# Optimization experiments

Measured on AMD Instinct MI355X. Metric: run time of the kernel, lower is better.

The kernel has to match this reference:

```python
import jax, jax.numpy as jnp
import numpy as np

N = 20000      # nodes per node type
E = 320000     # edges per relation (avg degree 16)
D_IN = 128     # input node feature dim
H = 256        # hidden_channels
L = 2          # num_layers
G = 32         # graphs in batch
NUM_REL = 6
# relation order: (vuln,ast,vuln),(vuln,dfg,vuln),(vuln,aligned,patch),(patch,aligned,vuln),(patch,ast,patch),(patch,dfg,patch)
REL_SRC = (0, 0, 0, 1, 1, 1)  # 0=vuln, 1=patch
REL_DST = (0, 0, 1, 0, 1, 1)


def setup_inputs() -> dict:
    key = jax.random.key(0)
    ks = jax.random.split(key, 12)
    s_in = 1.0 / np.sqrt(D_IN)
    s_h = 1.0 / np.sqrt(H)
    return {
        'x_vuln': jax.random.normal(ks[0], (N, D_IN), jnp.float32),
        'x_patch': jax.random.normal(ks[1], (N, D_IN), jnp.float32),
        'W_emb': jax.random.normal(ks[2], (2, D_IN, H), jnp.float32) * s_in,
        'b_emb': jnp.zeros((2, H), jnp.float32),
        'W_l': jax.random.normal(ks[3], (L, NUM_REL, H, H), jnp.float32) * s_h,
        'b_l': jnp.zeros((L, NUM_REL, H), jnp.float32),
        'W_r': jax.random.normal(ks[4], (L, NUM_REL, H, H), jnp.float32) * s_h,
        'gamma': jnp.ones((L, 2, H), jnp.float32),
        'beta': jnp.zeros((L, 2, H), jnp.float32),
        'W_out': jax.random.normal(ks[5], (2 * H, 1), jnp.float32) * (1.0 / np.sqrt(2 * H)),
        'b_out': jnp.zeros((1,), jnp.float32),
        'edge_index': jax.random.randint(ks[6], (NUM_REL, 2, E), 0, N, jnp.int64),
        'batch_vuln': jnp.sort(jax.random.randint(ks[7], (N,), 0, G, jnp.int64)),
        'batch_patch': jnp.sort(jax.random.randint(ks[8], (N,), 0, G, jnp.int64)),
        'num_graphs': G,
    }


def _segment_mean(data, seg, num):
    s = jax.ops.segment_sum(data, seg, num_segments=num)
    c = jax.ops.segment_sum(jnp.ones((data.shape[0], 1), data.dtype), seg, num_segments=num)
    return s / jnp.maximum(c, 1.0)


def _batchnorm(x, gamma, beta, eps=1e-5):
    m = x.mean(axis=0)
    v = x.var(axis=0)  # biased, matches torch BN normalization
    return (x - m) * jax.lax.rsqrt(v + eps) * gamma + beta


def reference(x_vuln, x_patch, W_emb, b_emb, W_l, b_l, W_r, gamma, beta,
              W_out, b_out, edge_index, batch_vuln, batch_patch, num_graphs):
    # per-type input projection
    xs = [x_vuln @ W_emb[0] + b_emb[0], x_patch @ W_emb[1] + b_emb[1]]
    n = [x_vuln.shape[0], x_patch.shape[0]]
    for i in range(L):
        prev = xs
        acc = [jnp.zeros((n[t], H), xs[0].dtype) for t in range(2)]
        cnt = [0, 0]
        for r in range(NUM_REL):  # fixed small structural loop over relations
            st, dt = REL_SRC[r], REL_DST[r]
            src, dst = edge_index[r, 0], edge_index[r, 1]
            agg = _segment_mean(xs[st][src], dst, n[dt])  # [n_dst, H] mean over in-neighbors
            out = agg @ W_l[i, r] + b_l[i, r] + xs[dt] @ W_r[i, r]  # SAGEConv
            acc[dt] = acc[dt] + out
            cnt[dt] += 1
        xs = [acc[t] / cnt[t] for t in range(2)]  # HeteroConv aggr='mean'
        xs = [jax.nn.relu(_batchnorm(xs[t], gamma[i, t], beta[i, t])) for t in range(2)]
        if i > 0:
            xs = [xs[t] + prev[t] for t in range(2)]  # residual
    gv = _segment_mean(xs[0], batch_vuln, num_graphs)   # global_mean_pool
    gp = _segment_mean(xs[1], batch_patch, num_graphs)
    cat = jnp.concatenate([gv, gp], axis=1)            # [G, 2H]
    return jax.nn.sigmoid(cat @ W_out + b_out)         # [G, 1]
```

## Files before the change

### kernel.cpp

```cpp
#include <hip/hip_runtime.h>
#include <math.h>

#define NODES 20000
#define EDGES 320000
#define DIN 128
#define HID 256
#define NGRAPH 32
#define NREL 6
#define STR 1088
#define NRG 32
#define RGN 625
#define BCAP 11264
#define BINSLC 4000

typedef __attribute__((ext_vector_type(8))) short bf16x8;
typedef __attribute__((ext_vector_type(8))) unsigned short u16x8;
typedef __attribute__((ext_vector_type(4))) unsigned short u16x4;
typedef __attribute__((ext_vector_type(4))) float f32x4;

__device__ __forceinline__ float bf2f(unsigned short u) {
  return __uint_as_float(((unsigned)u) << 16);
}
__device__ __forceinline__ unsigned short f2bf(float f) {
  unsigned u = __float_as_uint(f);
  unsigned r = (u + 0x7fffu + ((u >> 16) & 1u)) >> 16;
  return (unsigned short)r;
}

__device__ __forceinline__ unsigned char f2fp8(float f) {
  unsigned u = __float_as_uint(f);
  unsigned s = (u >> 24) & 0x80u;
  unsigned a = u & 0x7fffffffu;
  if (a < 0x3c800000u) return (unsigned char)s;
  if (a > 0x43e00000u) a = 0x43e00000u;
  a += 0x7ffffu + ((a >> 20) & 1u);
  unsigned em = (a >> 20) - (120u << 3);
  if (em > 0x7eu) em = 0x7eu;
  return (unsigned char)(s | em);
}
__device__ __forceinline__ float fp82f(unsigned b) {
  unsigned u = ((b & 0x80u) << 24) | ((b & 0x7fu) << 20);
  return __uint_as_float(u) * __uint_as_float(0x7B800000u);
}
__device__ __forceinline__ void fp8x4_acc(unsigned v, float& a0, float& a1, float& a2,
                                          float& a3) {
#if __has_builtin(__builtin_amdgcn_cvt_pk_f32_fp8)
  typedef float f32x2 __attribute__((ext_vector_type(2)));
  f32x2 lo = __builtin_amdgcn_cvt_pk_f32_fp8((int)v, false);
  f32x2 hi = __builtin_amdgcn_cvt_pk_f32_fp8((int)v, true);
  a0 += lo[0];
  a1 += lo[1];
  a2 += hi[0];
  a3 += hi[1];
#else
  a0 += fp82f(v & 0xffu);
  a1 += fp82f((v >> 8) & 0xffu);
  a2 += fp82f((v >> 16) & 0xffu);
  a3 += fp82f(v >> 24);
#endif
}

#define GLDS(g, l)                                                            \
  __builtin_amdgcn_global_load_lds(                                           \
      (const __attribute__((address_space(1))) void*)(g),                     \
      (__attribute__((address_space(3))) void*)(l), 16, 0, 0)

__global__ __launch_bounds__(256) void k_bin(const int* __restrict__ edges,
                                             unsigned* __restrict__ bucket,
                                             int* __restrict__ gcur) {
  __shared__ unsigned buf[NRG][256];
  __shared__ int cnt[NRG];
  __shared__ int gbaseL[NRG];
  int rel = blockIdx.y;
  for (int i = threadIdx.x; i < NRG; i += 256) cnt[i] = 0;
  __syncthreads();
  const int* srcp = edges + (size_t)rel * 2 * EDGES;
  const int* dstp = srcp + EDGES;
  int base = blockIdx.x * BINSLC;
  for (int i = base + threadIdx.x; i < base + BINSLC; i += 256) {
    int d = __builtin_nontemporal_load(&dstp[i]);
    int s = __builtin_nontemporal_load(&srcp[i]);
    int rg = (unsigned)d / RGN;
    int dl = d - rg * RGN;
    int p = atomicAdd(&cnt[rg], 1);
    if (p < 256) buf[rg][p] = ((unsigned)dl << 16) | (unsigned)s;
  }
  __syncthreads();
  if (threadIdx.x < NRG) {
    int n = min(cnt[threadIdx.x], 256);
    gbaseL[threadIdx.x] = atomicAdd(&gcur[rel * NRG + threadIdx.x], n);
    cnt[threadIdx.x] = n;
  }
  __syncthreads();
  for (int b = 0; b < NRG; ++b) {
    int n = cnt[b];
    unsigned* gb = bucket + ((size_t)rel * NRG + b) * BCAP + gbaseL[b];
    for (int k = threadIdx.x; k < n; k += 256) gb[k] = buf[b][k];
  }
}

__global__ void k_base(const int* __restrict__ gcur, int* __restrict__ gbase,
                       int* __restrict__ rowoff) {
  int t = threadIdx.x;
  for (int rel = 0; rel < NREL; ++rel) {
    int v = (t < NRG) ? gcur[rel * NRG + t] : 0;
    int x = v;
#pragma unroll
    for (int s = 1; s < NRG; s <<= 1) {
      int u = __shfl_up(x, s, 64);
      if (t >= s) x += u;
    }
    if (t < NRG) gbase[rel * NRG + t] = x - v;
    if (t == 0) rowoff[rel * (NODES + 1) + NODES] = EDGES;
  }
}

__global__ __launch_bounds__(256) void k_scat2(const unsigned* __restrict__ bucket,
                                               const int* __restrict__ gcur,
                                               const int* __restrict__ gbase,
                                               int* __restrict__ rowoff,
                                               unsigned short* __restrict__ csr16) {
  __shared__ int h[RGN];
  __shared__ int wsum[4];
  int rg = blockIdx.x, rel = blockIdx.y;
  int nE = gcur[rel * NRG + rg];
  int base = gbase[rel * NRG + rg];
  for (int i = threadIdx.x; i < RGN; i += 256) h[i] = 0;
  __syncthreads();
  const unsigned* bk = bucket + ((size_t)rel * NRG + rg) * BCAP;
  for (int i = threadIdx.x; i < nE; i += 256) atomicAdd(&h[bk[i] >> 16], 1);
  __syncthreads();
  int t = threadIdx.x, lane = t & 63, w = t >> 6;
  int i0 = t * 3;
  int v0 = (i0 < RGN) ? h[i0] : 0;
  int v1 = (i0 + 1 < RGN) ? h[i0 + 1] : 0;
  int v2 = (i0 + 2 < RGN) ? h[i0 + 2] : 0;
  int ts = v0 + v1 + v2;
  int x = ts;
#pragma unroll
  for (int s = 1; s < 64; s <<= 1) {
    int u = __shfl_up(x, s, 64);
    if (lane >= s) x += u;
  }
  if (lane == 63) wsum[w] = x;
  __syncthreads();
  int wb = 0;
  for (int k = 0; k < w; ++k) wb += wsum[k];
  int excl = base + wb + x - ts;
  int* ro = rowoff + rel * (NODES + 1) + rg * RGN;
  __syncthreads();
  if (i0 < RGN) {
    ro[i0] = excl;
    h[i0] = excl;
  }
  if (i0 + 1 < RGN) {
    ro[i0 + 1] = excl + v0;
    h[i0 + 1] = excl + v0;
  }
  if (i0 + 2 < RGN) {
    ro[i0 + 2] = excl + v0 + v1;
    h[i0 + 2] = excl + v0 + v1;
  }
  __syncthreads();
  unsigned short* cs = csr16 + (size_t)rel * EDGES;
  for (int i = threadIdx.x; i < nE; i += 256) {
    unsigned e = bk[i];
    int p = atomicAdd(&h[e >> 16], 1);
    cs[p] = (unsigned short)(e & 0xffffu);
  }
}

__global__ void k_xcvt(const float* __restrict__ xv, const float* __restrict__ xp,
                       unsigned short* __restrict__ xbf) {
  int idx = blockIdx.x * 256 + threadIdx.x;
  const int ND = NODES * DIN;
  int e0 = idx * 4;
  if (e0 >= 2 * ND) return;
  const float* s = (e0 < ND) ? (xv + e0) : (xp + e0 - ND);
  float4 v = *(const float4*)s;
  u16x4 o;
  o[0] = f2bf(v.x);
  o[1] = f2bf(v.y);
  o[2] = f2bf(v.z);
  o[3] = f2bf(v.w);
  *(u16x4*)(xbf + e0) = o;
}

__global__ void k_wtrans(const float* __restrict__ W_l, const float* __restrict__ W_r,
                         unsigned short* __restrict__ Wt) {
  const int rels[2][3] = {{0, 1, 3}, {2, 4, 5}};
  int kt = blockIdx.x, nt = blockIdx.y, ld = blockIdx.z;
  int layer = ld >> 1, dt = ld & 1;
  __shared__ float sh[16][17];
  int k0 = kt * 16, n0 = nt * 16;
  int seg = k0 >> 8, kk0 = k0 & 255;
  int tx = threadIdx.x, ty = threadIdx.y;
  float v;
  if (seg < 3) {
    v = W_l[(((size_t)layer * NREL + rels[dt][seg]) * HID + kk0 + ty) * HID + n0 + tx];
  } else {
    v = 0.f;
    for (int j = 0; j < 3; ++j)
      v += W_r[(((size_t)layer * NREL + rels[dt][j]) * HID + kk0 + ty) * HID + n0 + tx];
  }
  sh[ty][tx] = v;
  __syncthreads();
  Wt[((size_t)ld * HID + n0 + ty) * 1024 + k0 + tx] = f2bf(sh[tx][ty]);
}

__global__ void k_wembt(const float* __restrict__ W_emb, unsigned short* __restrict__ Wet) {
  int kt = blockIdx.x, nt = blockIdx.y, t = blockIdx.z;
  __shared__ float sh[16][17];
  int k0 = kt * 16, n0 = nt * 16;
  int tx = threadIdx.x, ty = threadIdx.y;
  sh[ty][tx] = W_emb[((size_t)t * DIN + k0 + ty) * HID + n0 + tx];
  __syncthreads();
  Wet[((size_t)t * HID + n0 + ty) * DIN + k0 + tx] = f2bf(sh[tx][ty]);
}

__global__ void k_bsum(const float* __restrict__ b_l, float* __restrict__ bsum) {
  const int rels[2][3] = {{0, 1, 3}, {2, 4, 5}};
  int idx = blockIdx.x * 256 + threadIdx.x;
  if (idx >= 1024) return;
  int layer = idx >> 9, dt = (idx >> 8) & 1, c = idx & 255;
  float s = 0.f;
  for (int j = 0; j < 3; ++j) s += b_l[(layer * NREL + rels[dt][j]) * HID + c];
  bsum[idx] = s;
}

__global__ __launch_bounds__(256) void k_agg(const unsigned char* __restrict__ xs8,
                                             unsigned short* __restrict__ a0,
                                             unsigned short* __restrict__ a1,
                                             const int* __restrict__ rowoff,
                                             const unsigned short* __restrict__ csr16) {
  const int dt_of[6] = {0, 0, 1, 0, 1, 1};
  const int seg_of[6] = {0, 1, 0, 2, 1, 2};
  int x = blockIdx.x;
  int st = x >> 2, rq = x & 3;
  int rel = st * 3 + blockIdx.z;
  int dt = dt_of[rel], seg = seg_of[rel];
  const unsigned char* src = xs8 + (size_t)st * NODES * 256;
  unsigned short* dstb = (dt == 0 ? a0 : a1) + seg * 256;
  int lane16 = threadIdx.x & 15;
  int rsub = threadIdx.x >> 4;
  unsigned coff = (unsigned)lane16 * 16u;
  const int* ro = rowoff + rel * (NODES + 1);
  const unsigned short* lst = csr16 + (size_t)rel * EDGES;
  int rlim = rq * 5000 + 5000;
  int rbase = rq * 5000 + blockIdx.y * 32;
#define LD(s) (*(const uint4*)(src + ((unsigned)(s) * 256u + coff)))
#define ACCV(v)                                  \
  {                                              \
    fp8x4_acc((v).x, ac[0], ac[1], ac[2], ac[3]);   \
    fp8x4_acc((v).y, ac[4], ac[5], ac[6], ac[7]);   \
    fp8x4_acc((v).z, ac[8], ac[9], ac[10], ac[11]); \
    fp8x4_acc((v).w, ac[12], ac[13], ac[14], ac[15]); \
  }
  int row = rbase + rsub;
  int o0 = 0, o1 = 0;
  if (row < rlim) {
    o0 = ro[row];
    o1 = ro[row + 1];
  }
#pragma unroll 1
  for (int pass = 0; pass < 2; ++pass) {
    int nrow = row + 16;
    int p0 = 0, p1 = 0;
    if (pass < 1 && nrow < rlim) {
      p0 = ro[nrow];
      p1 = ro[nrow + 1];
    }
    if (row < rlim) {
      float ac[16] = {};
      int nb = o1 - o0;
      int nfull = nb >> 2;
      int j = o0;
      if (nfull > 0) {
        unsigned idx[4];
#pragma unroll
        for (int b = 0; b < 4; ++b) idx[b] = (unsigned)lst[j + b];
#pragma unroll 1
        for (int f = 1;; ++f) {
          uint4 v0 = LD(idx[0]), v1 = LD(idx[1]), v2 = LD(idx[2]), v3 = LD(idx[3]);
          j += 4;
          bool more = (f < nfull);
          if (more) {
#pragma unroll
            for (int b = 0; b < 4; ++b) idx[b] = (unsigned)lst[j + b];
          }
          ACCV(v0);
          ACCV(v1);
          ACCV(v2);
          ACCV(v3);
          if (!more) break;
        }
      }
      int rem = nb & 3;
      if (rem & 2) {
        unsigned i0 = lst[j], i1 = lst[j + 1];
        uint4 v0 = LD(i0), v1 = LD(i1);
        ACCV(v0);
        ACCV(v1);
        j += 2;
      }
      if (rem & 1) {
        uint4 v0 = LD((unsigned)lst[j]);
        ACCV(v0);
      }
      float inv = nb ? 1.f / (float)nb : 0.f;
      u16x8 oa, ob;
#pragma unroll
      for (int e = 0; e < 8; ++e) {
        oa[e] = f2bf(ac[e] * inv);
        ob[e] = f2bf(ac[8 + e] * inv);
      }
      unsigned short* dp = dstb + (size_t)row * STR + lane16 * 16;
      *(u16x8*)dp = oa;
      *(u16x8*)(dp + 8) = ob;
    }
    row = nrow;
    o0 = p0;
    o1 = p1;
  }
#undef LD
#undef ACCV
}

template <int K, int AS, int OUTMODE>
__global__ __launch_bounds__(256) void k_mfma(const unsigned short* __restrict__ Abase,
                                              const unsigned short* __restrict__ Btbase,
                                              const float* __restrict__ biasbase,
                                              float* __restrict__ Crawbase,
                                              unsigned short* __restrict__ Cbfbase,
                                              unsigned char* __restrict__ X8base,
                                              float* __restrict__ statsbase) {
  int bid = blockIdx.x;
  int sel = blockIdx.y;
  int bm_i = (bid & 7) + 8 * (bid >> 5);
  int bn_i = (bid >> 3) & 3;
  if (bm_i >= 157) return;
  const unsigned short* A = Abase + (size_t)sel * NODES * AS;
  const unsigned short* Bt = Btbase + (size_t)sel * 256 * K;
  const float* bias = biasbase + sel * 256;
  const int bm = bm_i * 128, bn = bn_i * 64;
  __shared__ unsigned short As[2][128 * 64];
  __shared__ unsigned short Bs[2][64 * 64];
  const int tid = threadIdx.x, lane = tid & 63, w = tid >> 6;
  const int wr = w >> 1, wc = w & 1;
  const int srow = lane >> 3;
  const int schunk = lane & 7;
  const unsigned char* gA[4];
  const unsigned char* gB[2];
#pragma unroll
  for (int c = 0; c < 4; ++c) {
    int lr = 32 * c + w * 8 + srow;
    int r = bm + lr;
    if (r >= NODES) r = NODES - 1;
    gA[c] = (const unsigned char*)A + (size_t)r * AS * 2 + ((schunk ^ (lr & 7)) * 16);
  }
#pragma unroll
  for (int c = 0; c < 2; ++c) {
    int lr = 32 * c + w * 8 + srow;
    gB[c] = (const unsigned char*)Bt + (size_t)(bn + lr) * K * 2 + ((schunk ^ (lr & 7)) * 16);
  }

  auto stage = [&](int b, int k0) {
#pragma unroll
    for (int c = 0; c < 4; ++c) GLDS(gA[c] + 2 * k0, (char*)As[b] + c * 4096 + w * 1024);
#pragma unroll
    for (int c = 0; c < 2; ++c) GLDS(gB[c] + 2 * k0, (char*)Bs[b] + c * 4096 + w * 1024);
  };

  f32x4 acc[4][2] = {};
  stage(0, 0);
  __syncthreads();
  int cur = 0;
  for (int k0 = 0; k0 < K; k0 += 64) {
    if (k0 + 64 < K) stage(cur ^ 1, k0 + 64);
    const unsigned short* Ab = As[cur];
    const unsigned short* Bb = Bs[cur];
#pragma unroll
    for (int ks = 0; ks < 2; ++ks) {
      const int ci = ks * 4 + (lane >> 4);
      bf16x8 bfr[2];
#pragma unroll
      for (int n = 0; n < 2; ++n) {
        int rb = wc * 32 + n * 16 + (lane & 15);
        bfr[n] = *(const bf16x8*)((const char*)Bb + rb * 128 + ((ci ^ (rb & 7)) * 16));
      }
#pragma unroll
      for (int m = 0; m < 4; ++m) {
        int ra = wr * 64 + m * 16 + (lane & 15);
        bf16x8 afr = *(const bf16x8*)((const char*)Ab + ra * 128 + ((ci ^ (ra & 7)) * 16));
        acc[m][0] =
            __builtin_amdgcn_mfma_f32_16x16x32_bf16(afr, bfr[0], acc[m][0], 0, 0, 0);
        acc[m][1] =
            __builtin_amdgcn_mfma_f32_16x16x32_bf16(afr, bfr[1], acc[m][1], 0, 0, 0);
      }
    }
    __syncthreads();
    cur ^= 1;
  }

#pragma unroll
  for (int n = 0; n < 2; ++n) {
    int col = bn + wc * 32 + n * 16 + (lane & 15);
    float bv = bias[col];
    float s = 0.f, s2 = 0.f;
#pragma unroll
    for (int m = 0; m < 4; ++m) {
#pragma unroll
      for (int q = 0; q < 4; ++q) {
        int row = bm + wr * 64 + m * 16 + ((lane >> 4) * 4) + q;
        if (row < NODES) {
          float v = acc[m][n][q] + bv;
          if (OUTMODE == 0) {
            Crawbase[(size_t)sel * NODES * 256 + (size_t)row * 256 + col] = v;
            s += v;
            s2 = fmaf(v, v, s2);
          } else {
            Cbfbase[(size_t)sel * NODES * STR + (size_t)row * STR + col] = f2bf(v);
            X8base[(size_t)sel * NODES * 256 + (size_t)row * 256 + col] = f2fp8(v);
          }
        }
      }
    }
    if (OUTMODE == 0) {
      s += __shfl_xor(s, 16);
      s += __shfl_xor(s, 32);
      s2 += __shfl_xor(s2, 16);
      s2 += __shfl_xor(s2, 32);
      if (lane < 16) {
        float* stats = statsbase + sel * 512;
        atomicAdd(&stats[col], s);
        atomicAdd(&stats[256 + col], s2);
      }
    }
  }
}

__global__ __launch_bounds__(256) void k_bnapply(const float* __restrict__ rawbase,
                                                 const float* __restrict__ statsbase,
                                                 const float* __restrict__ gammabase,
                                                 const float* __restrict__ betabase,
                                                 unsigned short* __restrict__ outbase,
                                                 unsigned char* __restrict__ out8base) {
  int idx = blockIdx.x * 256 + threadIdx.x;
  if (idx >= NODES * 256) return;
  int dt = blockIdx.y;
  const float* raw = rawbase + (size_t)dt * NODES * 256;
  const float* stats = statsbase + dt * 512;
  const float* gamma = gammabase + dt * 256;
  const float* beta = betabase + dt * 256;
  unsigned short* out = outbase + (size_t)dt * NODES * STR;
  unsigned char* out8 = out8base + (size_t)dt * NODES * 256;
  int c = idx & 255;
  int rrow = idx >> 8;
  const float inv3 = 1.f / 3.f;
  float m = stats[c] * (inv3 / NODES);
  float ex2 = stats[256 + c] * (inv3 * inv3 / NODES);
  float var = ex2 - m * m;
  float v = (raw[idx] * inv3 - m) * rsqrtf(var + 1e-5f) * gamma[c] + beta[c];
  v = fmaxf(v, 0.f);
  out[(size_t)rrow * STR + c] = f2bf(v);
  out8[idx] = f2fp8(v);
}

__global__ __launch_bounds__(256) void k_pool(const float* __restrict__ rawbase,
                                              const float* __restrict__ statsbase,
                                              const float* __restrict__ gammabase,
                                              const float* __restrict__ betabase,
                                              const unsigned short* __restrict__ prevbase,
                                              const int* __restrict__ batch_v,
                                              const int* __restrict__ batch_p,
                                              float* __restrict__ pooledbase,
                                              float* __restrict__ gcntbase) {
  int dt = blockIdx.y;
  const float* raw = rawbase + (size_t)dt * NODES * 256;
  const float* stats = statsbase + dt * 512;
  const float* gamma = gammabase + dt * 256;
  const float* beta = betabase + dt * 256;
  const unsigned short* prev = prevbase + (size_t)dt * NODES * STR;
  const int* batch = dt ? batch_p : batch_v;
  float* pooled = pooledbase + dt * NGRAPH * 256;
  float* gcnt = gcntbase + dt * NGRAPH;
  int c = threadIdx.x;
  int rows_per = (NODES + gridDim.x - 1) / gridDim.x;
  int r0 = blockIdx.x * rows_per;
  int r1 = min(NODES, r0 + rows_per);
  if (r0 >= NODES) return;
  const float inv3 = 1.f / 3.f;
  float m = stats[c] * (inv3 / NODES);
  float ex2 = stats[256 + c] * (inv3 * inv3 / NODES);
  float rs = rsqrtf(ex2 - m * m + 1e-5f) * gamma[c];
  float bt = beta[c];
  float s = 0.f;
  int curg = batch[r0];
  for (int r = r0; r < r1; ++r) {
    int g = batch[r];
    if (g != curg) {
      atomicAdd(&pooled[curg * 256 + c], s);
      s = 0.f;
      curg = g;
    }
    float v = fmaxf((raw[(size_t)r * 256 + c] * inv3 - m) * rs + bt, 0.f) +
              bf2f(prev[(size_t)r * STR + c]);
    s += v;
  }
  atomicAdd(&pooled[curg * 256 + c], s);
  if (c == 0) {
    int cn = 0;
    int cg = batch[r0];
    for (int r = r0; r < r1; ++r) {
      int g = batch[r];
      if (g != cg) {
        atomicAdd(&gcnt[cg], (float)cn);
        cn = 0;
        cg = g;
      }
      cn++;
    }
    atomicAdd(&gcnt[cg], (float)cn);
  }
}

__global__ __launch_bounds__(256) void k_final(const float* __restrict__ pooled,
                                               const float* __restrict__ gcnt,
                                               const float* __restrict__ Wout,
                                               const float* __restrict__ bout,
                                               float* __restrict__ out) {
  int g = blockIdx.x;
  int h = threadIdx.x;
  float cv = fmaxf(gcnt[g], 1.f);
  float cp = fmaxf(gcnt[NGRAPH + g], 1.f);
  float v = pooled[g * 256 + h] / cv * Wout[h] +
            pooled[NGRAPH * 256 + g * 256 + h] / cp * Wout[256 + h];
#pragma unroll
  for (int s = 32; s > 0; s >>= 1) v += __shfl_down(v, s, 64);
  __shared__ float sh[4];
  if ((h & 63) == 0) sh[h >> 6] = v;
  __syncthreads();
  if (h == 0) {
    float t = sh[0] + sh[1] + sh[2] + sh[3] + bout[0];
    out[g] = 1.f / (1.f + expf(-t));
  }
}

extern "C" void kernel_launch(void* const* d_in, const int* in_sizes, int n_in,
                              void* d_out, int out_size, void* d_ws, size_t ws_size,
                              hipStream_t stream) {
  const float* x_vuln = (const float*)d_in[0];
  const float* x_patch = (const float*)d_in[1];
  const float* W_emb = (const float*)d_in[2];
  const float* b_emb = (const float*)d_in[3];
  const float* W_l = (const float*)d_in[4];
  const float* b_l = (const float*)d_in[5];
  const float* W_r = (const float*)d_in[6];
  const float* gamma = (const float*)d_in[7];
  const float* beta = (const float*)d_in[8];
  const float* W_out = (const float*)d_in[9];
  const float* b_out = (const float*)d_in[10];
  const int* edge_index = (const int*)d_in[11];
  const int* batch_vuln = (const int*)d_in[12];
  const int* batch_patch = (const int*)d_in[13];

  char* ws = (char*)d_ws;
  size_t off = 0;
  auto alloc = [&](size_t bytes) -> void* {
    void* p = ws + off;
    off = (off + bytes + 255) & ~(size_t)255;
    return p;
  };
  unsigned short* csr16 = (unsigned short*)alloc((size_t)NREL * EDGES * 2);
  int* rowoff = (int*)alloc((size_t)NREL * (NODES + 1) * 4);
  unsigned short* Acat[2];
  Acat[0] = (unsigned short*)alloc((size_t)NODES * STR * 2);
  Acat[1] = (unsigned short*)alloc((size_t)NODES * STR * 2);
  float* raw[2];
  raw[0] = (float*)alloc((size_t)NODES * 256 * 4);
  raw[1] = (float*)alloc((size_t)NODES * 256 * 4);
  unsigned char* xs8 = (unsigned char*)alloc((size_t)2 * NODES * 256);
  unsigned short* xbf = (unsigned short*)alloc((size_t)2 * NODES * DIN * 2);
  unsigned short* Wt = (unsigned short*)alloc((size_t)4 * 256 * 1024 * 2);
  unsigned short* Wet = (unsigned short*)alloc((size_t)2 * 256 * DIN * 2);
  float* bsum = (float*)alloc(1024 * 4);
  unsigned* bucket = (unsigned*)raw[0];
  int* gbase = (int*)alloc((size_t)NREL * NRG * 4);
  size_t zoff0 = off;
  int* gcur = (int*)alloc((size_t)NREL * NRG * 4);
  float* stats = (float*)alloc((size_t)2 * 2 * 512 * 4);
  float* pooled = (float*)alloc((size_t)2 * NGRAPH * 256 * 4);
  float* gcnt = (float*)alloc((size_t)2 * NGRAPH * 4);
  size_t zbytes = off - zoff0;
  hipMemsetAsync(ws + zoff0, 0, zbytes, stream);

  k_bin<<<dim3(EDGES / BINSLC, NREL), 256, 0, stream>>>(edge_index, bucket, gcur);
  k_base<<<1, 64, 0, stream>>>(gcur, gbase, rowoff);
  k_scat2<<<dim3(NRG, NREL), 256, 0, stream>>>(bucket, gcur, gbase, rowoff, csr16);

  k_xcvt<<<(2 * NODES * DIN / 4 + 255) / 256, 256, 0, stream>>>(x_vuln, x_patch, xbf);
  k_wtrans<<<dim3(64, 16, 4), dim3(16, 16), 0, stream>>>(W_l, W_r, Wt);
  k_wembt<<<dim3(8, 16, 2), dim3(16, 16), 0, stream>>>(W_emb, Wet);
  k_bsum<<<4, 256, 0, stream>>>(b_l, bsum);

  k_mfma<DIN, DIN, 1><<<dim3(640, 2), 256, 0, stream>>>(xbf, Wet, b_emb, nullptr,
                                                        Acat[0] + 768, xs8, nullptr);

  for (int layer = 0; layer < 2; ++layer) {
    k_agg<<<dim3(8, 157, 3), 256, 0, stream>>>(xs8, Acat[0], Acat[1], rowoff, csr16);
    k_mfma<1024, STR, 0><<<dim3(640, 2), 256, 0, stream>>>(
        Acat[0], Wt + (size_t)layer * 2 * 256 * 1024, bsum + layer * 512, raw[0],
        nullptr, nullptr, stats + layer * 1024);
    if (layer == 0)
      k_bnapply<<<dim3((NODES * 256 + 255) / 256, 2), 256, 0, stream>>>(
          raw[0], stats, gamma, beta, Acat[0] + 768, xs8);
  }

  k_pool<<<dim3(128, 2), 256, 0, stream>>>(raw[0], stats + 2 * 512, gamma + 2 * 256,
                                           beta + 2 * 256, Acat[0] + 768, batch_vuln,
                                           batch_patch, pooled, gcnt);
  k_final<<<NGRAPH, 256, 0, stream>>>(pooled, gcnt, W_out, b_out, (float*)d_out);
}
```

Baseline: 361.4 us.

## Shrink MFMA K-tile to 32 and store raw layer output as bf16

The GEMM kernel now stages 32-wide K slices instead of 64 and adjusts the LDS swizzle to match. This halves shared memory per block, which should allow more resident blocks, at the cost of twice as many barriers per K loop. Separately, the pre-BatchNorm raw output is written as bf16 instead of fp32, and the BN-apply and pooling kernels read it back as bf16. That halves the traffic for this intermediate, while statistics are still accumulated in fp32 before rounding, so a small precision loss is introduced in the normalized values.

```diff
diff --git a/kernel.cpp b/kernel.cpp
--- a/kernel.cpp
+++ b/kernel.cpp
@@ -330,7 +330,7 @@
 __global__ __launch_bounds__(256) void k_mfma(const unsigned short* __restrict__ Abase,
                                               const unsigned short* __restrict__ Btbase,
                                               const float* __restrict__ biasbase,
-                                              float* __restrict__ Crawbase,
+                                              unsigned short* __restrict__ Crawbase,
                                               unsigned short* __restrict__ Cbfbase,
                                               unsigned char* __restrict__ X8base,
                                               float* __restrict__ statsbase) {
@@ -343,60 +343,55 @@
   const unsigned short* Bt = Btbase + (size_t)sel * 256 * K;
   const float* bias = biasbase + sel * 256;
   const int bm = bm_i * 128, bn = bn_i * 64;
-  __shared__ unsigned short As[2][128 * 64];
-  __shared__ unsigned short Bs[2][64 * 64];
+  __shared__ unsigned short As[2][128 * 32];
+  __shared__ unsigned short Bs[2][64 * 32];
   const int tid = threadIdx.x, lane = tid & 63, w = tid >> 6;
   const int wr = w >> 1, wc = w & 1;
-  const int srow = lane >> 3;
-  const int schunk = lane & 7;
-  const unsigned char* gA[4];
-  const unsigned char* gB[2];
-#pragma unroll
-  for (int c = 0; c < 4; ++c) {
-    int lr = 32 * c + w * 8 + srow;
+  const int srow = lane >> 2;
+  const int schunk = lane & 3;
+  const unsigned char* gA[2];
+  const unsigned char* gB;
+#pragma unroll
+  for (int c = 0; c < 2; ++c) {
+    int lr = c * 64 + w * 16 + srow;
     int r = bm + lr;
     if (r >= NODES) r = NODES - 1;
-    gA[c] = (const unsigned char*)A + (size_t)r * AS * 2 + ((schunk ^ (lr & 7)) * 16);
-  }
-#pragma unroll
-  for (int c = 0; c < 2; ++c) {
-    int lr = 32 * c + w * 8 + srow;
-    gB[c] = (const unsigned char*)Bt + (size_t)(bn + lr) * K * 2 + ((schunk ^ (lr & 7)) * 16);
+    gA[c] = (const unsigned char*)A + (size_t)r * AS * 2 +
+            ((schunk ^ ((lr >> 1) & 3)) * 16);
+  }
+  {
+    int lr = w * 16 + srow;
+    gB = (const unsigned char*)Bt + (size_t)(bn + lr) * K * 2 +
+         ((schunk ^ ((lr >> 1) & 3)) * 16);
   }
 
   auto stage = [&](int b, int k0) {
-#pragma unroll
-    for (int c = 0; c < 4; ++c) GLDS(gA[c] + 2 * k0, (char*)As[b] + c * 4096 + w * 1024);
-#pragma unroll
-    for (int c = 0; c < 2; ++c) GLDS(gB[c] + 2 * k0, (char*)Bs[b] + c * 4096 + w * 1024);
+    GLDS(gA[0] + 2 * k0, (char*)As[b] + w * 1024);
+    GLDS(gA[1] + 2 * k0, (char*)As[b] + 4096 + w * 1024);
+    GLDS(gB + 2 * k0, (char*)Bs[b] + w * 1024);
   };
 
   f32x4 acc[4][2] = {};
+  const int ci = lane >> 4;
   stage(0, 0);
   __syncthreads();
   int cur = 0;
-  for (int k0 = 0; k0 < K; k0 += 64) {
-    if (k0 + 64 < K) stage(cur ^ 1, k0 + 64);
+  for (int k0 = 0; k0 < K; k0 += 32) {
+    if (k0 + 32 < K) stage(cur ^ 1, k0 + 32);
     const unsigned short* Ab = As[cur];
     const unsigned short* Bb = Bs[cur];
-#pragma unroll
-    for (int ks = 0; ks < 2; ++ks) {
-      const int ci = ks * 4 + (lane >> 4);
-      bf16x8 bfr[2];
-#pragma unroll
-      for (int n = 0; n < 2; ++n) {
-        int rb = wc * 32 + n * 16 + (lane & 15);
-        bfr[n] = *(const bf16x8*)((const char*)Bb + rb * 128 + ((ci ^ (rb & 7)) * 16));
-      }
-#pragma unroll
-      for (int m = 0; m < 4; ++m) {
-        int ra = wr * 64 + m * 16 + (lane & 15);
-        bf16x8 afr = *(const bf16x8*)((const char*)Ab + ra * 128 + ((ci ^ (ra & 7)) * 16));
-        acc[m][0] =
-            __builtin_amdgcn_mfma_f32_16x16x32_bf16(afr, bfr[0], acc[m][0], 0, 0, 0);
-        acc[m][1] =
-            __builtin_amdgcn_mfma_f32_16x16x32_bf16(afr, bfr[1], acc[m][1], 0, 0, 0);
-      }
+    bf16x8 bfr[2];
+#pragma unroll
+    for (int n = 0; n < 2; ++n) {
+      int rb = wc * 32 + n * 16 + (lane & 15);
+      bfr[n] = *(const bf16x8*)((const char*)Bb + rb * 64 + ((ci ^ ((rb >> 1) & 3)) * 16));
+    }
+#pragma unroll
+    for (int m = 0; m < 4; ++m) {
+      int ra = wr * 64 + m * 16 + (lane & 15);
+      bf16x8 afr = *(const bf16x8*)((const char*)Ab + ra * 64 + ((ci ^ ((ra >> 1) & 3)) * 16));
+      acc[m][0] = __builtin_amdgcn_mfma_f32_16x16x32_bf16(afr, bfr[0], acc[m][0], 0, 0, 0);
+      acc[m][1] = __builtin_amdgcn_mfma_f32_16x16x32_bf16(afr, bfr[1], acc[m][1], 0, 0, 0);
     }
     __syncthreads();
     cur ^= 1;
@@ -415,7 +410,7 @@
         if (row < NODES) {
           float v = acc[m][n][q] + bv;
           if (OUTMODE == 0) {
-            Crawbase[(size_t)sel * NODES * 256 + (size_t)row * 256 + col] = v;
+            Crawbase[(size_t)sel * NODES * 256 + (size_t)row * 256 + col] = f2bf(v);
             s += v;
             s2 = fmaf(v, v, s2);
           } else {
@@ -439,7 +434,7 @@
   }
 }
 
-__global__ __launch_bounds__(256) void k_bnapply(const float* __restrict__ rawbase,
+__global__ __launch_bounds__(256) void k_bnapply(const unsigned short* __restrict__ rawbase,
                                                  const float* __restrict__ statsbase,
                                                  const float* __restrict__ gammabase,
                                                  const float* __restrict__ betabase,
@@ -448,7 +443,7 @@
   int idx = blockIdx.x * 256 + threadIdx.x;
   if (idx >= NODES * 256) return;
   int dt = blockIdx.y;
-  const float* raw = rawbase + (size_t)dt * NODES * 256;
+  const unsigned short* raw = rawbase + (size_t)dt * NODES * 256;
   const float* stats = statsbase + dt * 512;
   const float* gamma = gammabase + dt * 256;
   const float* beta = betabase + dt * 256;
@@ -460,13 +455,13 @@
   float m = stats[c] * (inv3 / NODES);
   float ex2 = stats[256 + c] * (inv3 * inv3 / NODES);
   float var = ex2 - m * m;
-  float v = (raw[idx] * inv3 - m) * rsqrtf(var + 1e-5f) * gamma[c] + beta[c];
+  float v = (bf2f(raw[idx]) * inv3 - m) * rsqrtf(var + 1e-5f) * gamma[c] + beta[c];
   v = fmaxf(v, 0.f);
   out[(size_t)rrow * STR + c] = f2bf(v);
   out8[idx] = f2fp8(v);
 }
 
-__global__ __launch_bounds__(256) void k_pool(const float* __restrict__ rawbase,
+__global__ __launch_bounds__(256) void k_pool(const unsigned short* __restrict__ rawbase,
                                               const float* __restrict__ statsbase,
                                               const float* __restrict__ gammabase,
                                               const float* __restrict__ betabase,
@@ -476,7 +471,7 @@
                                               float* __restrict__ pooledbase,
                                               float* __restrict__ gcntbase) {
   int dt = blockIdx.y;
-  const float* raw = rawbase + (size_t)dt * NODES * 256;
+  const unsigned short* raw = rawbase + (size_t)dt * NODES * 256;
   const float* stats = statsbase + dt * 512;
   const float* gamma = gammabase + dt * 256;
   const float* beta = betabase + dt * 256;
@@ -503,7 +498,7 @@
       s = 0.f;
       curg = g;
     }
-    float v = fmaxf((raw[(size_t)r * 256 + c] * inv3 - m) * rs + bt, 0.f) +
+    float v = fmaxf((bf2f(raw[(size_t)r * 256 + c]) * inv3 - m) * rs + bt, 0.f) +
               bf2f(prev[(size_t)r * STR + c]);
     s += v;
   }
@@ -576,15 +571,13 @@
   unsigned short* Acat[2];
   Acat[0] = (unsigned short*)alloc((size_t)NODES * STR * 2);
   Acat[1] = (unsigned short*)alloc((size_t)NODES * STR * 2);
-  float* raw[2];
-  raw[0] = (float*)alloc((size_t)NODES * 256 * 4);
-  raw[1] = (float*)alloc((size_t)NODES * 256 * 4);
+  unsigned short* rawbf = (unsigned short*)alloc((size_t)2 * NODES * 256 * 2);
   unsigned char* xs8 = (unsigned char*)alloc((size_t)2 * NODES * 256);
   unsigned short* xbf = (unsigned short*)alloc((size_t)2 * NODES * DIN * 2);
   unsigned short* Wt = (unsigned short*)alloc((size_t)4 * 256 * 1024 * 2);
   unsigned short* Wet = (unsigned short*)alloc((size_t)2 * 256 * DIN * 2);
   float* bsum = (float*)alloc(1024 * 4);
-  unsigned* bucket = (unsigned*)raw[0];
+  unsigned* bucket = (unsigned*)rawbf;
   int* gbase = (int*)alloc((size_t)NREL * NRG * 4);
   size_t zoff0 = off;
   int* gcur = (int*)alloc((size_t)NREL * NRG * 4);
@@ -609,14 +602,14 @@
   for (int layer = 0; layer < 2; ++layer) {
     k_agg<<<dim3(8, 157, 3), 256, 0, stream>>>(xs8, Acat[0], Acat[1], rowoff, csr16);
     k_mfma<1024, STR, 0><<<dim3(640, 2), 256, 0, stream>>>(
-        Acat[0], Wt + (size_t)layer * 2 * 256 * 1024, bsum + layer * 512, raw[0],
+        Acat[0], Wt + (size_t)layer * 2 * 256 * 1024, bsum + layer * 512, rawbf,
         nullptr, nullptr, stats + layer * 1024);
     if (layer == 0)
       k_bnapply<<<dim3((NODES * 256 + 255) / 256, 2), 256, 0, stream>>>(
-          raw[0], stats, gamma, beta, Acat[0] + 768, xs8);
-  }
-
-  k_pool<<<dim3(128, 2), 256, 0, stream>>>(raw[0], stats + 2 * 512, gamma + 2 * 256,
+          rawbf, stats, gamma, beta, Acat[0] + 768, xs8);
+  }
+
+  k_pool<<<dim3(128, 2), 256, 0, stream>>>(rawbf, stats + 2 * 512, gamma + 2 * 256,
                                            beta + 2 * 256, Acat[0] + 768, batch_vuln,
                                            batch_patch, pooled, gcnt);
   k_final<<<NGRAPH, 256, 0, stream>>>(pooled, gcnt, W_out, b_out, (float*)d_out);
```

Result: no change. 358.0 us (-0.9%).
